# Optimization experiments

Measured on AMD Instinct MI355X. Metric: run time of the kernel, lower is better.

Reference implementation:

```python
import jax, jax.numpy as jnp
import numpy as np

B, HH, WW = 4, 192, 192
DIM, HEADS, WIN, SHIFT, HID = 256, 8, 8, 4, 1024
EPS = 1e-5


def _rel_index(w):
    coords = np.stack(np.meshgrid(np.arange(w), np.arange(w), indexing='ij')).reshape(2, -1)
    rel = coords[:, :, None] - coords[:, None, :]            # [2, N, N]
    rel = rel.transpose(1, 2, 0).astype(np.int64)
    rel[:, :, 0] += w - 1
    rel[:, :, 1] += w - 1
    rel[:, :, 0] *= 2 * w - 1
    return rel.sum(-1)                                        # [N, N]


def _ln(x, g, b):
    m = x.mean(-1, keepdims=True)
    v = ((x - m) ** 2).mean(-1, keepdims=True)
    return (x - m) / jnp.sqrt(v + EPS) * g + b


def setup_inputs() -> dict:
    key = jax.random.key(0)
    ks = jax.random.split(key, 8)
    s = 0.02
    return {
        'x': jax.random.normal(ks[0], (B, HH * WW, DIM), jnp.float32),
        'norm1_g': jnp.ones((DIM,), jnp.float32),
        'norm1_b': jnp.zeros((DIM,), jnp.float32),
        'qkv_w': s * jax.random.normal(ks[1], (DIM, 3 * DIM), jnp.float32),
        'qkv_b': jnp.zeros((3 * DIM,), jnp.float32),
        'bias_table': s * jax.random.normal(ks[2], ((2 * WIN - 1) ** 2, HEADS), jnp.float32),
        'proj_w': s * jax.random.normal(ks[3], (DIM, DIM), jnp.float32),
        'proj_b': jnp.zeros((DIM,), jnp.float32),
        'norm2_g': jnp.ones((DIM,), jnp.float32),
        'norm2_b': jnp.zeros((DIM,), jnp.float32),
        'fc1_w': s * jax.random.normal(ks[4], (DIM, HID), jnp.float32),
        'fc1_b': jnp.zeros((HID,), jnp.float32),
        'fc2_w': s * jax.random.normal(ks[5], (HID, DIM), jnp.float32),
        'fc2_b': jnp.zeros((DIM,), jnp.float32),
        'H': HH,
        'W': WW,
    }


def reference(x, norm1_g, norm1_b, qkv_w, qkv_b, bias_table, proj_w, proj_b,
              norm2_g, norm2_b, fc1_w, fc1_b, fc2_w, fc2_b, H, W):
    Bn, L, C = x.shape
    hd = C // HEADS
    win = min(WIN, H, W)
    shift = SHIFT if win > SHIFT else 0
    shortcut = x

    h = _ln(x, norm1_g, norm1_b).reshape(Bn, H, W, C)
    pad_b = (win - H % win) % win
    pad_r = (win - W % win) % win
    h = jnp.pad(h, ((0, 0), (0, pad_b), (0, pad_r), (0, 0)))
    Hp, Wp = H + pad_b, W + pad_r
    if shift > 0:
        h = jnp.roll(h, (-shift, -shift), axis=(1, 2))

    nh, nw = Hp // win, Wp // win
    h = h.reshape(Bn, nh, win, nw, win, C).transpose(0, 1, 3, 2, 4, 5)
    h = h.reshape(Bn * nh * nw, win * win, C)
    N = win * win

    # windowed attention
    qkv = (h @ qkv_w + qkv_b).reshape(-1, N, 3, HEADS, hd)
    q, k, v = qkv[:, :, 0], qkv[:, :, 1], qkv[:, :, 2]      # [Bw, N, H, hd]
    scale = hd ** -0.5
    attn = jnp.einsum('bqhd,bkhd->bhqk', q * scale, k)
    rel_idx = jnp.asarray(_rel_index(win))                   # [N, N]
    bias = bias_table[rel_idx.reshape(-1)].reshape(N, N, HEADS).transpose(2, 0, 1)
    attn = jax.nn.softmax(attn + bias[None], axis=-1)
    o = jnp.einsum('bhqk,bkhd->bqhd', attn, v).reshape(-1, N, C)
    o = o @ proj_w + proj_b

    # window reverse
    o = o.reshape(Bn, nh, nw, win, win, C).transpose(0, 1, 3, 2, 4, 5).reshape(Bn, Hp, Wp, C)
    if shift > 0:
        o = jnp.roll(o, (shift, shift), axis=(1, 2))
    o = o[:, :H, :W, :].reshape(Bn, H * W, C)

    x = shortcut + o
    m = _ln(x, norm2_g, norm2_b)
    m = jax.nn.gelu(m @ fc1_w + fc1_b, approximate=False) @ fc2_w + fc2_b
    return x + m
```

## Files before the change

### kernel.cpp

```cpp
#include <hip/hip_runtime.h>


#define SHIFT_ 4

typedef __attribute__((ext_vector_type(8))) short short8;
typedef __attribute__((ext_vector_type(4))) float floatx4;

__device__ __forceinline__ float b2f(unsigned short u) {
  union { unsigned int i; float f; } c; c.i = ((unsigned int)u) << 16; return c.f;
}
__device__ __forceinline__ unsigned short f2b(float f) {
  union { float f; unsigned int i; } c; c.f = f;
  unsigned int u = c.i;
  return (unsigned short)((u + 0x7FFFu + ((u >> 16) & 1u)) >> 16);
}

__device__ __forceinline__ void load_lds16(const void* g, void* l) {
  __builtin_amdgcn_global_load_lds((__attribute__((address_space(1))) void*)g,
                                   (__attribute__((address_space(3))) void*)l, 16, 0, 0);
}

__device__ __forceinline__ size_t tok_of_row(int row) {
  int widx = row >> 6, t = row & 63;
  int b = widx / 576; int rem = widx - b * 576;
  int wy = rem / 24, wx = rem - wy * 24;
  int ti = t >> 3, tj = t & 7;
  int gr = wy * 8 + ti + SHIFT_; if (gr >= 192) gr -= 192;
  int gc = wx * 8 + tj + SHIFT_; if (gc >= 192) gc -= 192;
  return (size_t)b * 36864 + (size_t)(gr * 192 + gc);
}

template<int SHUFFLE>
__global__ __launch_bounds__(256) void ln_kernel(const float* __restrict__ src,
    const float* __restrict__ gw, const float* __restrict__ bw,
    unsigned short* __restrict__ dst) {
  const int lane = threadIdx.x & 63;
  const int m = blockIdx.x * 4 + (threadIdx.x >> 6);
  const size_t soff = SHUFFLE ? tok_of_row(m) * 256 : (size_t)m * 256;
  float4 xv = *(const float4*)(src + soff + lane * 4);
  float s  = xv.x + xv.y + xv.z + xv.w;
  float s2 = xv.x * xv.x + xv.y * xv.y + xv.z * xv.z + xv.w * xv.w;
  #pragma unroll
  for (int off = 32; off > 0; off >>= 1) { s += __shfl_xor(s, off); s2 += __shfl_xor(s2, off); }
  const float mean = s * 0.00390625f;
  const float var  = s2 * 0.00390625f - mean * mean;
  const float rstd = rsqrtf(var + 1e-5f);
  float4 gv = *(const float4*)(gw + lane * 4);
  float4 bv = *(const float4*)(bw + lane * 4);
  ushort4 o;
  o.x = f2b((xv.x - mean) * rstd * gv.x + bv.x);
  o.y = f2b((xv.y - mean) * rstd * gv.y + bv.y);
  o.z = f2b((xv.z - mean) * rstd * gv.z + bv.z);
  o.w = f2b((xv.w - mean) * rstd * gv.w + bv.w);
  *(ushort4*)(dst + (size_t)m * 256 + lane * 4) = o;
}

__global__ void wconv(const float* __restrict__ W, unsigned short* __restrict__ Wt,
                      int K, int N) {
  const int idx = blockIdx.x * 256 + threadIdx.x;
  const int n = idx / K, k = idx - n * K;
  Wt[idx] = f2b(W[(size_t)k * N + n]);
}

template<int MODE>
__global__ __launch_bounds__(256) void gemm_bt(
    const unsigned short* __restrict__ A, const unsigned short* __restrict__ Wt,
    const float* __restrict__ bias, const float* __restrict__ X,
    unsigned short* __restrict__ outb, float* __restrict__ outf,
    int Ntot, int K) {
  __shared__ unsigned short sm[8192];
  const int tid = threadIdx.x;
  const int wave = tid >> 6, lane = tid & 63;
  const int lr = lane & 15, lg = lane >> 4;
  const int wm = wave >> 1, wn = wave & 1;
  const int m0 = blockIdx.y * 128, n0 = blockIdx.x * 128;
  floatx4 acc[4][4];
  #pragma unroll
  for (int i = 0; i < 4; ++i)
    #pragma unroll
    for (int j = 0; j < 4; ++j) acc[i][j] = (floatx4)0.f;

  for (int k0 = 0; k0 < K; k0 += 32) {
    __syncthreads();
    #pragma unroll
    for (int t = 0; t < 4; ++t) {
      const int chunk = wave * 4 + t;
      const int eoff = chunk * 512 + lane * 8;
      const unsigned short* gp;
      if (chunk < 8) {
        const int r = eoff >> 5, c = eoff & 31;
        gp = A + (size_t)(m0 + r) * K + (k0 + c);
      } else {
        const int e = eoff - 4096;
        const int r = e >> 5, c = e & 31;
        gp = Wt + (size_t)(n0 + r) * K + (k0 + c);
      }
      load_lds16(gp, &sm[chunk * 512]);
    }
    __syncthreads();
    short8 af[4], bf[4];
    #pragma unroll
    for (int mi = 0; mi < 4; ++mi)
      af[mi] = *(const short8*)&sm[(wm * 64 + mi * 16 + lr) * 32 + lg * 8];
    #pragma unroll
    for (int ni = 0; ni < 4; ++ni)
      bf[ni] = *(const short8*)&sm[4096 + (wn * 64 + ni * 16 + lr) * 32 + lg * 8];
    #pragma unroll
    for (int mi = 0; mi < 4; ++mi)
      #pragma unroll
      for (int ni = 0; ni < 4; ++ni)
        acc[mi][ni] = __builtin_amdgcn_mfma_f32_16x16x32_bf16(af[mi], bf[ni], acc[mi][ni], 0, 0, 0);
  }

  #pragma unroll
  for (int mi = 0; mi < 4; ++mi) {
    #pragma unroll
    for (int r = 0; r < 4; ++r) {
      const int row = m0 + wm * 64 + mi * 16 + lg * 4 + r;
      size_t obase;
      if (MODE == 1) obase = tok_of_row(row) * 256;
      else obase = (size_t)row * Ntot;
      #pragma unroll
      for (int ni = 0; ni < 4; ++ni) {
        const int col = n0 + wn * 64 + ni * 16 + lr;
        const float v = acc[mi][ni][r] + bias[col];
        if (MODE == 0) {
          outb[obase + col] = f2b(v);
        } else if (MODE == 1) {
          outf[obase + col] = X[obase + col] + v;
        } else if (MODE == 2) {
          outb[obase + col] = f2b(0.5f * v * (1.f + erff(v * 0.70710678f)));
        } else {
          outf[obase + col] = X[obase + col] + v;
        }
      }
    }
  }
}

__global__ __launch_bounds__(64) void attn_kernel(const unsigned short* __restrict__ qkv,
    const float* __restrict__ btab, unsigned short* __restrict__ obuf) {
  __shared__ unsigned short qs[2048];
  __shared__ unsigned short ks[2048];
  __shared__ unsigned short vts[2048];
  __shared__ unsigned short ps[4096];
  __shared__ float bs[225];
  const int l = threadIdx.x;
  const int win = blockIdx.x >> 3, head = blockIdx.x & 7;
  const int lr = l & 15, lg = l >> 4;
  const unsigned short* base = qkv + (size_t)(win * 64 + l) * 768 + head * 32;
  #pragma unroll
  for (int c = 0; c < 4; ++c) {
    *(uint4*)&qs[l * 32 + c * 8] = *(const uint4*)(base + c * 8);
    *(uint4*)&ks[l * 32 + c * 8] = *(const uint4*)(base + 256 + c * 8);
  }
  #pragma unroll
  for (int c = 0; c < 8; ++c) {
    ushort4 vv = *(const ushort4*)(base + 512 + c * 4);
    vts[(c * 4 + 0) * 64 + l] = vv.x;
    vts[(c * 4 + 1) * 64 + l] = vv.y;
    vts[(c * 4 + 2) * 64 + l] = vv.z;
    vts[(c * 4 + 3) * 64 + l] = vv.w;
  }
  for (int i = l; i < 225; i += 64) bs[i] = btab[i * 8 + head];
  __syncthreads();

  short8 af[4], bfr[4];
  #pragma unroll
  for (int mi = 0; mi < 4; ++mi) af[mi] = *(const short8*)&qs[(mi * 16 + lr) * 32 + lg * 8];
  #pragma unroll
  for (int ni = 0; ni < 4; ++ni) bfr[ni] = *(const short8*)&ks[(ni * 16 + lr) * 32 + lg * 8];
  floatx4 sa[4][4];
  #pragma unroll
  for (int mi = 0; mi < 4; ++mi)
    #pragma unroll
    for (int ni = 0; ni < 4; ++ni)
      sa[mi][ni] = __builtin_amdgcn_mfma_f32_16x16x32_bf16(af[mi], bfr[ni], (floatx4)0.f, 0, 0, 0);

  const float scale = 0.17677669529663687f;
  #pragma unroll
  for (int mi = 0; mi < 4; ++mi) {
    #pragma unroll
    for (int r = 0; r < 4; ++r) {
      const int qi = mi * 16 + lg * 4 + r;
      const int ti = qi >> 3, tj = qi & 7;
      float vals[4];
      #pragma unroll
      for (int ni = 0; ni < 4; ++ni) {
        const int kc = ni * 16 + lr;
        const int tk = kc >> 3, tl = kc & 7;
        vals[ni] = sa[mi][ni][r] * scale + bs[(ti - tk + 7) * 15 + (tj - tl + 7)];
      }
      float mx = fmaxf(fmaxf(vals[0], vals[1]), fmaxf(vals[2], vals[3]));
      #pragma unroll
      for (int off = 1; off < 16; off <<= 1) mx = fmaxf(mx, __shfl_xor(mx, off, 16));
      float se = 0.f;
      #pragma unroll
      for (int ni = 0; ni < 4; ++ni) { vals[ni] = __expf(vals[ni] - mx); se += vals[ni]; }
      #pragma unroll
      for (int off = 1; off < 16; off <<= 1) se += __shfl_xor(se, off, 16);
      const float inv = 1.f / se;
      #pragma unroll
      for (int ni = 0; ni < 4; ++ni) ps[qi * 64 + ni * 16 + lr] = f2b(vals[ni] * inv);
    }
  }
  __syncthreads();

  floatx4 oa[4][2];
  #pragma unroll
  for (int mi = 0; mi < 4; ++mi) { oa[mi][0] = (floatx4)0.f; oa[mi][1] = (floatx4)0.f; }
  #pragma unroll
  for (int kk = 0; kk < 2; ++kk) {
    short8 pa[4], vb[2];
    #pragma unroll
    for (int mi = 0; mi < 4; ++mi) pa[mi] = *(const short8*)&ps[(mi * 16 + lr) * 64 + kk * 32 + lg * 8];
    #pragma unroll
    for (int nj = 0; nj < 2; ++nj) vb[nj] = *(const short8*)&vts[(nj * 16 + lr) * 64 + kk * 32 + lg * 8];
    #pragma unroll
    for (int mi = 0; mi < 4; ++mi)
      #pragma unroll
      for (int nj = 0; nj < 2; ++nj)
        oa[mi][nj] = __builtin_amdgcn_mfma_f32_16x16x32_bf16(pa[mi], vb[nj], oa[mi][nj], 0, 0, 0);
  }
  #pragma unroll
  for (int mi = 0; mi < 4; ++mi)
    #pragma unroll
    for (int nj = 0; nj < 2; ++nj)
      #pragma unroll
      for (int r = 0; r < 4; ++r) {
        const int row = mi * 16 + lg * 4 + r, d = nj * 16 + lr;
        obuf[(size_t)(win * 64 + row) * 256 + head * 32 + d] = f2b(oa[mi][nj][r]);
      }
}

extern "C" void kernel_launch(void* const* d_in, const int* in_sizes, int n_in,
                              void* d_out, int out_size, void* d_ws, size_t ws_size,
                              hipStream_t stream) {
  (void)in_sizes; (void)n_in; (void)out_size; (void)ws_size;
  const float* x      = (const float*)d_in[0];
  const float* n1g    = (const float*)d_in[1];
  const float* n1b    = (const float*)d_in[2];
  const float* qkv_w  = (const float*)d_in[3];
  const float* qkv_b  = (const float*)d_in[4];
  const float* btab   = (const float*)d_in[5];
  const float* proj_w = (const float*)d_in[6];
  const float* proj_b = (const float*)d_in[7];
  const float* n2g    = (const float*)d_in[8];
  const float* n2b    = (const float*)d_in[9];
  const float* fc1_w  = (const float*)d_in[10];
  const float* fc1_b  = (const float*)d_in[11];
  const float* fc2_w  = (const float*)d_in[12];
  const float* fc2_b  = (const float*)d_in[13];
  float* out = (float*)d_out;

  char* wsb = (char*)d_ws;
  unsigned short* wqkv  = (unsigned short*)(wsb);
  unsigned short* wproj = (unsigned short*)(wsb + 393216);
  unsigned short* wfc1  = (unsigned short*)(wsb + 524288);
  unsigned short* wfc2  = (unsigned short*)(wsb + 1048576);
  unsigned short* hbuf  = (unsigned short*)(wsb + 1572864);
  unsigned short* big   = (unsigned short*)(wsb + 77070336);

  wconv<<<768, 256, 0, stream>>>(qkv_w, wqkv, 256, 768);
  wconv<<<256, 256, 0, stream>>>(proj_w, wproj, 256, 256);
  wconv<<<1024, 256, 0, stream>>>(fc1_w, wfc1, 256, 1024);
  wconv<<<1024, 256, 0, stream>>>(fc2_w, wfc2, 1024, 256);

  ln_kernel<1><<<36864, 256, 0, stream>>>(x, n1g, n1b, hbuf);
  gemm_bt<0><<<dim3(6, 1152), 256, 0, stream>>>(hbuf, wqkv, qkv_b, nullptr, big, nullptr, 768, 256);
  attn_kernel<<<18432, 64, 0, stream>>>(big, btab, hbuf);
  gemm_bt<1><<<dim3(2, 1152), 256, 0, stream>>>(hbuf, wproj, proj_b, x, nullptr, out, 256, 256);
  ln_kernel<0><<<36864, 256, 0, stream>>>(out, n2g, n2b, hbuf);
  gemm_bt<2><<<dim3(8, 1152), 256, 0, stream>>>(hbuf, wfc1, fc1_b, nullptr, big, nullptr, 1024, 256);
  gemm_bt<3><<<dim3(2, 1152), 256, 0, stream>>>(big, wfc2, fc2_b, out, nullptr, out, 256, 1024);
}
```

Measured before the change: 1.047 ms.

## Swizzle LDS layouts, widen GEMM K-step, load attention Q/K fragments directly

```diff
diff --git a/kernel.cpp b/kernel.cpp
--- a/kernel.cpp
+++ b/kernel.cpp
@@ -6,9 +6,6 @@
 typedef __attribute__((ext_vector_type(8))) short short8;
 typedef __attribute__((ext_vector_type(4))) float floatx4;
 
-__device__ __forceinline__ float b2f(unsigned short u) {
-  union { unsigned int i; float f; } c; c.i = ((unsigned int)u) << 16; return c.f;
-}
 __device__ __forceinline__ unsigned short f2b(float f) {
   union { float f; unsigned int i; } c; c.f = f;
   unsigned int u = c.i;
@@ -68,7 +65,7 @@
     const float* __restrict__ bias, const float* __restrict__ X,
     unsigned short* __restrict__ outb, float* __restrict__ outf,
     int Ntot, int K) {
-  __shared__ unsigned short sm[8192];
+  __shared__ unsigned short sm[16384];
   const int tid = threadIdx.x;
   const int wave = tid >> 6, lane = tid & 63;
   const int lr = lane & 15, lg = lane >> 4;
@@ -80,36 +77,43 @@
     #pragma unroll
     for (int j = 0; j < 4; ++j) acc[i][j] = (floatx4)0.f;
 
-  for (int k0 = 0; k0 < K; k0 += 32) {
+  for (int k0 = 0; k0 < K; k0 += 64) {
     __syncthreads();
     #pragma unroll
-    for (int t = 0; t < 4; ++t) {
-      const int chunk = wave * 4 + t;
-      const int eoff = chunk * 512 + lane * 8;
+    for (int t = 0; t < 8; ++t) {
+      const int chunk = wave * 8 + t;
       const unsigned short* gp;
-      if (chunk < 8) {
-        const int r = eoff >> 5, c = eoff & 31;
-        gp = A + (size_t)(m0 + r) * K + (k0 + c);
+      if (chunk < 16) {
+        const int P = chunk * 64 + lane;
+        const int r = P >> 3, pc = P & 7, c = pc ^ (r & 7);
+        gp = A + (size_t)(m0 + r) * K + (k0 + c * 8);
       } else {
-        const int e = eoff - 4096;
-        const int r = e >> 5, c = e & 31;
-        gp = Wt + (size_t)(n0 + r) * K + (k0 + c);
+        const int P = chunk * 64 + lane - 1024;
+        const int r = P >> 3, pc = P & 7, c = pc ^ (r & 7);
+        gp = Wt + (size_t)(n0 + r) * K + (k0 + c * 8);
       }
       load_lds16(gp, &sm[chunk * 512]);
     }
     __syncthreads();
-    short8 af[4], bf[4];
-    #pragma unroll
-    for (int mi = 0; mi < 4; ++mi)
-      af[mi] = *(const short8*)&sm[(wm * 64 + mi * 16 + lr) * 32 + lg * 8];
-    #pragma unroll
-    for (int ni = 0; ni < 4; ++ni)
-      bf[ni] = *(const short8*)&sm[4096 + (wn * 64 + ni * 16 + lr) * 32 + lg * 8];
-    #pragma unroll
-    for (int mi = 0; mi < 4; ++mi)
-      #pragma unroll
-      for (int ni = 0; ni < 4; ++ni)
-        acc[mi][ni] = __builtin_amdgcn_mfma_f32_16x16x32_bf16(af[mi], bf[ni], acc[mi][ni], 0, 0, 0);
+    #pragma unroll
+    for (int kk = 0; kk < 2; ++kk) {
+      short8 af[4], bf[4];
+      #pragma unroll
+      for (int mi = 0; mi < 4; ++mi) {
+        const int r = wm * 64 + mi * 16 + lr;
+        af[mi] = *(const short8*)&sm[r * 64 + (((kk * 4 + lg) ^ (r & 7)) * 8)];
+      }
+      #pragma unroll
+      for (int ni = 0; ni < 4; ++ni) {
+        const int r = wn * 64 + ni * 16 + lr;
+        bf[ni] = *(const short8*)&sm[8192 + r * 64 + (((kk * 4 + lg) ^ (r & 7)) * 8)];
+      }
+      #pragma unroll
+      for (int mi = 0; mi < 4; ++mi)
+        #pragma unroll
+        for (int ni = 0; ni < 4; ++ni)
+          acc[mi][ni] = __builtin_amdgcn_mfma_f32_16x16x32_bf16(af[mi], bf[ni], acc[mi][ni], 0, 0, 0);
+    }
   }
 
   #pragma unroll
@@ -140,42 +144,42 @@
 
 __global__ __launch_bounds__(64) void attn_kernel(const unsigned short* __restrict__ qkv,
     const float* __restrict__ btab, unsigned short* __restrict__ obuf) {
-  __shared__ unsigned short qs[2048];
-  __shared__ unsigned short ks[2048];
   __shared__ unsigned short vts[2048];
   __shared__ unsigned short ps[4096];
   __shared__ float bs[225];
   const int l = threadIdx.x;
   const int win = blockIdx.x >> 3, head = blockIdx.x & 7;
   const int lr = l & 15, lg = l >> 4;
-  const unsigned short* base = qkv + (size_t)(win * 64 + l) * 768 + head * 32;
-  #pragma unroll
-  for (int c = 0; c < 4; ++c) {
-    *(uint4*)&qs[l * 32 + c * 8] = *(const uint4*)(base + c * 8);
-    *(uint4*)&ks[l * 32 + c * 8] = *(const uint4*)(base + 256 + c * 8);
-  }
+  const unsigned short* base = qkv + (size_t)(win * 64) * 768 + head * 32;
+
   #pragma unroll
   for (int c = 0; c < 8; ++c) {
-    ushort4 vv = *(const ushort4*)(base + 512 + c * 4);
-    vts[(c * 4 + 0) * 64 + l] = vv.x;
-    vts[(c * 4 + 1) * 64 + l] = vv.y;
-    vts[(c * 4 + 2) * 64 + l] = vv.z;
-    vts[(c * 4 + 3) * 64 + l] = vv.w;
+    ushort4 vv = *(const ushort4*)(base + (size_t)l * 768 + 512 + c * 4);
+    #pragma unroll
+    for (int j = 0; j < 4; ++j) {
+      const int d = c * 4 + j;
+      const unsigned short val = j == 0 ? vv.x : j == 1 ? vv.y : j == 2 ? vv.z : vv.w;
+      vts[d * 64 + (((l >> 3) ^ (d & 7)) * 8) + (l & 7)] = val;
+    }
   }
   for (int i = l; i < 225; i += 64) bs[i] = btab[i * 8 + head];
-  __syncthreads();
 
   short8 af[4], bfr[4];
   #pragma unroll
-  for (int mi = 0; mi < 4; ++mi) af[mi] = *(const short8*)&qs[(mi * 16 + lr) * 32 + lg * 8];
-  #pragma unroll
-  for (int ni = 0; ni < 4; ++ni) bfr[ni] = *(const short8*)&ks[(ni * 16 + lr) * 32 + lg * 8];
+  for (int mi = 0; mi < 4; ++mi)
+    af[mi] = *(const short8*)(base + (size_t)(mi * 16 + lr) * 768 + lg * 8);
+  #pragma unroll
+  for (int ni = 0; ni < 4; ++ni)
+    bfr[ni] = *(const short8*)(base + (size_t)(ni * 16 + lr) * 768 + 256 + lg * 8);
+
   floatx4 sa[4][4];
   #pragma unroll
   for (int mi = 0; mi < 4; ++mi)
     #pragma unroll
     for (int ni = 0; ni < 4; ++ni)
       sa[mi][ni] = __builtin_amdgcn_mfma_f32_16x16x32_bf16(af[mi], bfr[ni], (floatx4)0.f, 0, 0, 0);
+
+  __syncthreads();
 
   const float scale = 0.17677669529663687f;
   #pragma unroll
@@ -201,7 +205,11 @@
       for (int off = 1; off < 16; off <<= 1) se += __shfl_xor(se, off, 16);
       const float inv = 1.f / se;
       #pragma unroll
-      for (int ni = 0; ni < 4; ++ni) ps[qi * 64 + ni * 16 + lr] = f2b(vals[ni] * inv);
+      for (int ni = 0; ni < 4; ++ni) {
+        const int col = ni * 16 + lr;
+        const int cell = col >> 3;
+        ps[qi * 64 + ((cell ^ (qi & 7)) * 8) + (col & 7)] = f2b(vals[ni] * inv);
+      }
     }
   }
   __syncthreads();
@@ -213,9 +221,15 @@
   for (int kk = 0; kk < 2; ++kk) {
     short8 pa[4], vb[2];
     #pragma unroll
-    for (int mi = 0; mi < 4; ++mi) pa[mi] = *(const short8*)&ps[(mi * 16 + lr) * 64 + kk * 32 + lg * 8];
-    #pragma unroll
-    for (int nj = 0; nj < 2; ++nj) vb[nj] = *(const short8*)&vts[(nj * 16 + lr) * 64 + kk * 32 + lg * 8];
+    for (int mi = 0; mi < 4; ++mi) {
+      const int r = mi * 16 + lr;
+      pa[mi] = *(const short8*)&ps[r * 64 + (((kk * 4 + lg) ^ (r & 7)) * 8)];
+    }
+    #pragma unroll
+    for (int nj = 0; nj < 2; ++nj) {
+      const int r = nj * 16 + lr;
+      vb[nj] = *(const short8*)&vts[r * 64 + (((kk * 4 + lg) ^ (r & 7)) * 8)];
+    }
     #pragma unroll
     for (int mi = 0; mi < 4; ++mi)
       #pragma unroll
```

New measurement: 970.3 us. -7.3%, faster.
